# Performance work log

Measured on AMD Instinct MI355X. Metric: run time of the kernel, lower is better.

The kernel has to match this reference:

```python
import jax, jax.numpy as jnp
import numpy as np

N_NODES = 100_000
N_EDGES = 1_600_000
N_GRAPHS = 1024
IN_CH = 5
EPS_BN = 1e-5


def _p(key, shape, scale=0.1):
    return scale * jax.random.normal(key, shape, dtype=jnp.float32)


def setup_inputs() -> dict:
    key = jax.random.key(0)
    ks = jax.random.split(key, 24)
    x = jax.random.normal(ks[0], (N_NODES, IN_CH), dtype=jnp.float32)
    edge_index = jax.random.randint(ks[1], (2, N_EDGES), 0, N_NODES, dtype=jnp.int64)
    batch = jnp.sort(jax.random.randint(ks[2], (N_NODES,), 0, N_GRAPHS, dtype=jnp.int64))
    return {
        "x": x, "edge_index": edge_index, "batch": batch,
        "W1": _p(ks[3], (IN_CH, 128)), "a1_src": _p(ks[4], (4, 32)), "a1_dst": _p(ks[5], (4, 32)), "b1": jnp.zeros((128,), jnp.float32),
        "g1": jnp.ones((128,), jnp.float32), "be1": jnp.zeros((128,), jnp.float32),
        "W2": _p(ks[6], (128, 128)), "a2_src": _p(ks[7], (4, 32)), "a2_dst": _p(ks[8], (4, 32)), "b2": jnp.zeros((128,), jnp.float32),
        "g2": jnp.ones((128,), jnp.float32), "be2": jnp.zeros((128,), jnp.float32),
        # conv3: 128 -> 64, 1 head, mean (concat=False)
        "W3": _p(ks[9], (128, 64)), "a3_src": _p(ks[10], (1, 64)), "a3_dst": _p(ks[11], (1, 64)), "b3": jnp.zeros((64,), jnp.float32),
        # classifier Linear(128,64) -> ELU -> Linear(64,1)
        "fc1_w": _p(ks[12], (128, 64)), "fc1_b": jnp.zeros((64,), jnp.float32),
        "fc2_w": _p(ks[13], (64, 1)), "fc2_b": jnp.zeros((1,), jnp.float32),
    }


def _gat_conv(x, src, dst, W, a_src, a_dst, bias, heads, out_ch, concat):
    """PyG GATConv (negative_slope=0.2, self-loops already appended, eval-mode dropout)."""
    n = x.shape[0]
    h = (x @ W).reshape(n, heads, out_ch)                      # [N,H,C]
    al_s = jnp.sum(h * a_src, axis=-1)                         # [N,H]
    al_d = jnp.sum(h * a_dst, axis=-1)                         # [N,H]
    e = jax.nn.leaky_relu(al_s[src] + al_d[dst], 0.2)          # [E,H]
    m = jax.lax.stop_gradient(jax.ops.segment_max(e, dst, num_segments=n))
    p = jnp.exp(e - m[dst])
    s = jax.ops.segment_sum(p, dst, num_segments=n)
    alpha = p / (s[dst] + 1e-16)                               # segment softmax over in-edges of dst
    out = jax.ops.segment_sum(h[src] * alpha[:, :, None], dst, num_segments=n)  # [N,H,C]
    out = out.reshape(n, heads * out_ch) if concat else out.mean(axis=1)
    return out + bias


def _bn(x, g, b):
    mu = x.mean(axis=0)
    var = x.var(axis=0)
    return (x - mu) * jax.lax.rsqrt(var + EPS_BN) * g + b


def reference(x, edge_index, batch,
              W1, a1_src, a1_dst, b1, g1, be1,
              W2, a2_src, a2_dst, b2, g2, be2,
              W3, a3_src, a3_dst, b3,
              fc1_w, fc1_b, fc2_w, fc2_b):
    n = x.shape[0]
    # PyG GATConv default add_self_loops=True
    loops = jnp.arange(n, dtype=edge_index.dtype)
    src = jnp.concatenate([edge_index[0], loops])
    dst = jnp.concatenate([edge_index[1], loops])

    h = jax.nn.elu(_bn(_gat_conv(x, src, dst, W1, a1_src, a1_dst, b1, 4, 32, True), g1, be1))
    h = jax.nn.elu(_bn(_gat_conv(h, src, dst, W2, a2_src, a2_dst, b2, 4, 32, True), g2, be2))
    h = jax.nn.elu(_gat_conv(h, src, dst, W3, a3_src, a3_dst, b3, 1, 64, False))  # [N,64]

    counts = jax.ops.segment_sum(jnp.ones((n,), h.dtype), batch, num_segments=N_GRAPHS)
    mean_p = jax.ops.segment_sum(h, batch, num_segments=N_GRAPHS) / jnp.maximum(counts, 1.0)[:, None]
    max_p = jax.ops.segment_max(h, batch, num_segments=N_GRAPHS)
    max_p = jnp.where(counts[:, None] > 0, max_p, 0.0)
    hg = jnp.concatenate([mean_p, max_p], axis=1)              # [B,128]

    z = jax.nn.elu(hg @ fc1_w + fc1_b)
    return (z @ fc2_w + fc2_b).squeeze(-1)                     # [B]
```

## Files before the change

### kernel.cpp

```cpp
#include <hip/hip_runtime.h>
#include <hip/hip_bf16.h>
#include <hip/hip_fp16.h>


#define BSHIFT 7
#define BCAP 4096
#define BUCKCAP 2560
#define SCH 32

typedef __attribute__((ext_vector_type(8))) _Float16 half8;
typedef __attribute__((ext_vector_type(4))) float f32x4;

__device__ __forceinline__ float leaky02(float e) { return e > 0.f ? e : 0.2f * e; }

__device__ __forceinline__ unsigned short f16u(float x) {
    __half h = __float2half_rn(x);
    return *(unsigned short*)&h;
}
__device__ __forceinline__ unsigned pack_h2(float a, float b) {
    __half2 h = __floats2half2_rn(a, b);
    return *(unsigned*)&h;
}
__device__ __forceinline__ float2 h2f2(unsigned u) {
    __half2 h = *(__half2*)&u;
    return __half22float2(h);
}

__global__ __launch_bounds__(256) void k_bscatter(const int* __restrict__ src,
                                                  const int* __restrict__ dst,
                                                  int* __restrict__ cursor,
                                                  uint2* __restrict__ ebuf, int E, int nb) {
    __shared__ int hist[1024];
    __shared__ int baseArr[1024];
    int tid = threadIdx.x;
    int chunk0 = blockIdx.x * (256 * SCH);
    for (int i = tid; i < nb; i += 256) hist[i] = 0;
    __syncthreads();
    int rank[SCH];
#pragma unroll
    for (int it = 0; it < SCH; it++) {
        int e = chunk0 + it * 256 + tid;
        rank[it] = (e < E) ? atomicAdd(&hist[dst[e] >> BSHIFT], 1) : 0;
    }
    __syncthreads();
    for (int b = tid; b < nb; b += 256) {
        int c = hist[b];
        baseArr[b] = c ? atomicAdd(&cursor[b], c) : 0;
    }
    __syncthreads();
#pragma unroll
    for (int it = 0; it < SCH; it++) {
        int e = chunk0 + it * 256 + tid;
        if (e < E) {
            int d = dst[e];
            int bk = d >> BSHIFT;
            int local = baseArr[bk] + rank[it];
            if (local < BUCKCAP)
                ebuf[(size_t)bk * BUCKCAP + local] = make_uint2((unsigned)d, (unsigned)src[e]);
        }
    }
}

__global__ __launch_bounds__(256) void k_bsort(const uint2* __restrict__ ebuf,
                                               const int* __restrict__ cursor,
                                               int2* __restrict__ rowInfo,
                                               int* __restrict__ colv, int N) {
    int b = blockIdx.x;
    int base = b * BUCKCAP;
    int count = cursor[b];
    if (count > BUCKCAP) count = BUCKCAP;
    int tid = threadIdx.x;
    __shared__ int hist[128], scanin[128], hist2[128];
    __shared__ int lrank[BCAP];
    __shared__ int lsrc[BCAP];
    if (tid < 128) { hist[tid] = 0; hist2[tid] = 0; }
    __syncthreads();
    bool staged = (count <= BCAP);
    for (int i = tid; i < count; i += 256) {
        uint2 p = ebuf[base + i];
        int local = p.x & 127;
        int r = atomicAdd(&hist[local], 1);
        if (staged) lrank[i] = (r << 7) | local;
    }
    __syncthreads();
    if (tid < 128) scanin[tid] = hist[tid];
    __syncthreads();
#pragma unroll
    for (int off = 1; off < 128; off <<= 1) {
        int v = 0;
        if (tid < 128 && tid >= off) v = scanin[tid - off];
        __syncthreads();
        if (tid < 128) scanin[tid] += v;
        __syncthreads();
    }
    int nodeBase = b << BSHIFT;
    if (tid < 128) {
        int n = nodeBase + tid;
        if (n < N) {
            int beg = base + scanin[tid] - hist[tid];
            rowInfo[n] = make_int2(beg, beg + hist[tid]);
        }
    }
    __syncthreads();
    if (staged) {
        for (int i = tid; i < count; i += 256) {
            uint2 p = ebuf[base + i];
            int lr = lrank[i];
            int local = lr & 127;
            int pos = (scanin[local] - hist[local]) + (lr >> 7);
            lsrc[pos] = (int)p.y;
        }
        __syncthreads();
        for (int i = tid; i < count; i += 256) colv[base + i] = lsrc[i];
    } else {
        for (int i = tid; i < count; i += 256) {
            uint2 p = ebuf[base + i];
            int local = p.x & 127;
            int r = atomicAdd(&hist2[local], 1);
            colv[base + (scanin[local] - hist[local]) + r] = (int)p.y;
        }
    }
}

__global__ __launch_bounds__(256) void k_l1(const float* __restrict__ x, const float* __restrict__ W,
                                            const float* __restrict__ asrc, const float* __restrict__ adst,
                                            unsigned* __restrict__ hb, float* __restrict__ als,
                                            float* __restrict__ ald, int N, int waveBlk,
                                            const float* __restrict__ W2, const float* __restrict__ W3,
                                            unsigned short* __restrict__ Wt2h,
                                            unsigned short* __restrict__ Wt3h) {
    if ((int)blockIdx.x >= waveBlk) {
        int which = blockIdx.x - waveBlk;
        const float* Wsrc = which ? W3 : W2;
        unsigned short* Wdst = which ? Wt3h : Wt2h;
        int sh = which ? 6 : 7;
        int total = 128 << sh;
        int msk = (1 << sh) - 1;
        for (int i = threadIdx.x; i < total; i += 256) {
            int k = i >> sh, n = i & msk;
            Wdst[n * 128 + k] = f16u(Wsrc[i]);
        }
        return;
    }
    int w = (blockIdx.x * blockDim.x + threadIdx.x) >> 6;
    if (w >= N) return;
    int lane = threadIdx.x & 63;
    float xv[5];
#pragma unroll
    for (int k = 0; k < 5; k++) xv[k] = x[(size_t)w * 5 + k];
    int c0 = 2 * lane;
    float h0 = 0.f, h1 = 0.f;
#pragma unroll
    for (int k = 0; k < 5; k++) {
        float2 wv = ((const float2*)(W + k * 128))[lane];
        h0 += xv[k] * wv.x;
        h1 += xv[k] * wv.y;
    }
    hb[(size_t)w * 64 + lane] = pack_h2(h0, h1);
    float s = h0 * asrc[c0] + h1 * asrc[c0 + 1];
    float d = h0 * adst[c0] + h1 * adst[c0 + 1];
#pragma unroll
    for (int off = 1; off <= 8; off <<= 1) { s += __shfl_xor(s, off); d += __shfl_xor(d, off); }
    if ((lane & 15) == 0) {
        int g = lane >> 4;
        als[(size_t)w * 4 + g] = s;
        ald[(size_t)w * 4 + g] = d;
    }
}

__global__ __launch_bounds__(256) void k_agg128(const unsigned* __restrict__ h,
                                                const float* __restrict__ als, const float* __restrict__ ald,
                                                const int2* __restrict__ rowInfo, const int* __restrict__ colv,
                                                const float* __restrict__ bias,
                                                unsigned* __restrict__ out, int N) {
    int w = (blockIdx.x * blockDim.x + threadIdx.x) >> 6;
    if (w >= N) return;
    int lane = threadIdx.x & 63;
    int grp = lane >> 4;
    int l16 = lane & 15;
    int head = l16 >> 2;
    float aldn = ald[(size_t)w * 4 + head];
    float acc[8] = {};
    float dsum = 0.f;

    auto edge = [&](int s) {
        float a = als[(size_t)s * 4 + head];
        float wt = __expf(leaky02(a + aldn));
        uint4 u = *(const uint4*)&h[(size_t)s * 64 + l16 * 4];
        float2 p0 = h2f2(u.x), p1 = h2f2(u.y), p2 = h2f2(u.z), p3 = h2f2(u.w);
        acc[0] += wt * p0.x; acc[1] += wt * p0.y;
        acc[2] += wt * p1.x; acc[3] += wt * p1.y;
        acc[4] += wt * p2.x; acc[5] += wt * p2.y;
        acc[6] += wt * p3.x; acc[7] += wt * p3.y;
        dsum += wt;
    };

    if (grp == 0) edge(w);
    int2 ri = rowInfo[w];
    int p = ri.x + grp, end = ri.y;
    for (; p + 4 < end; p += 8) {
        int s0 = colv[p], s1 = colv[p + 4];
        edge(s0);
        edge(s1);
    }
    if (p < end) edge(colv[p]);

#pragma unroll
    for (int i = 0; i < 8; i++) {
        acc[i] += __shfl_xor(acc[i], 16);
        acc[i] += __shfl_xor(acc[i], 32);
    }
    dsum += __shfl_xor(dsum, 16);
    dsum += __shfl_xor(dsum, 32);

    if (grp == 0) {
        float inv = 1.f / (dsum + 1e-16f);
        const float4* b4 = (const float4*)(bias + 8 * l16);
        float4 bv0 = b4[0], bv1 = b4[1];
        float v[8];
        v[0] = acc[0] * inv + bv0.x; v[1] = acc[1] * inv + bv0.y;
        v[2] = acc[2] * inv + bv0.z; v[3] = acc[3] * inv + bv0.w;
        v[4] = acc[4] * inv + bv1.x; v[5] = acc[5] * inv + bv1.y;
        v[6] = acc[6] * inv + bv1.z; v[7] = acc[7] * inv + bv1.w;
        uint4 o;
        o.x = pack_h2(v[0], v[1]);
        o.y = pack_h2(v[2], v[3]);
        o.z = pack_h2(v[4], v[5]);
        o.w = pack_h2(v[6], v[7]);
        *(uint4*)&out[(size_t)w * 64 + l16 * 4] = o;
    }
}

__global__ __launch_bounds__(256) void k_agg64(const unsigned* __restrict__ h,
                                               const float* __restrict__ als, const float* __restrict__ ald,
                                               const int2* __restrict__ rowInfo, const int* __restrict__ colv,
                                               const float* __restrict__ bias,
                                               unsigned* __restrict__ out, int N) {
    int w = (blockIdx.x * blockDim.x + threadIdx.x) >> 6;
    if (w >= N) return;
    int lane = threadIdx.x & 63;
    int grp = lane >> 3;
    int l8 = lane & 7;
    float aldn = ald[w];
    float acc[8] = {};
    float dsum = 0.f;

    auto edge = [&](int s) {
        float wt = __expf(leaky02(als[s] + aldn));
        uint4 u = *(const uint4*)&h[(size_t)s * 32 + l8 * 4];
        float2 p0 = h2f2(u.x), p1 = h2f2(u.y), p2 = h2f2(u.z), p3 = h2f2(u.w);
        acc[0] += wt * p0.x; acc[1] += wt * p0.y;
        acc[2] += wt * p1.x; acc[3] += wt * p1.y;
        acc[4] += wt * p2.x; acc[5] += wt * p2.y;
        acc[6] += wt * p3.x; acc[7] += wt * p3.y;
        dsum += wt;
    };

    if (grp == 0) edge(w);
    int2 ri = rowInfo[w];
    int p = ri.x + grp, end = ri.y;
    for (; p + 8 < end; p += 16) {
        int s0 = colv[p], s1 = colv[p + 8];
        edge(s0);
        edge(s1);
    }
    if (p < end) edge(colv[p]);

#pragma unroll
    for (int i = 0; i < 8; i++) {
        acc[i] += __shfl_xor(acc[i], 8);
        acc[i] += __shfl_xor(acc[i], 16);
        acc[i] += __shfl_xor(acc[i], 32);
    }
    dsum += __shfl_xor(dsum, 8);
    dsum += __shfl_xor(dsum, 16);
    dsum += __shfl_xor(dsum, 32);

    if (grp == 0) {
        float inv = 1.f / (dsum + 1e-16f);
        const float4* b4 = (const float4*)(bias + 8 * l8);
        float4 bv0 = b4[0], bv1 = b4[1];
        float v[8];
#pragma unroll
        for (int i = 0; i < 8; i++) v[i] = acc[i] * inv;
        v[0] += bv0.x; v[1] += bv0.y; v[2] += bv0.z; v[3] += bv0.w;
        v[4] += bv1.x; v[5] += bv1.y; v[6] += bv1.z; v[7] += bv1.w;
#pragma unroll
        for (int i = 0; i < 8; i++) v[i] = v[i] > 0.f ? v[i] : expm1f(v[i]);
        uint4 o;
        o.x = pack_h2(v[0], v[1]);
        o.y = pack_h2(v[2], v[3]);
        o.z = pack_h2(v[4], v[5]);
        o.w = pack_h2(v[6], v[7]);
        *(uint4*)&out[(size_t)w * 32 + l8 * 4] = o;
    }
}

__global__ __launch_bounds__(256) void k_bnstats_b(const unsigned* __restrict__ x,
                                                   float* __restrict__ stats, int N) {
    __shared__ float lsum[128], lsq[128];
    int tid = threadIdx.x;
    if (tid < 128) { lsum[tid] = 0.f; lsq[tid] = 0.f; }
    __syncthreads();
    int wrd = tid & 63;
    int part = tid >> 6;
    float s0 = 0.f, q0 = 0.f, s1 = 0.f, q1 = 0.f;
    for (int r = blockIdx.x * 4 + part; r < N; r += gridDim.x * 4) {
        float2 v = h2f2(x[(size_t)r * 64 + wrd]);
        s0 += v.x; q0 += v.x * v.x;
        s1 += v.y; q1 += v.y * v.y;
    }
    atomicAdd(&lsum[2 * wrd], s0);
    atomicAdd(&lsum[2 * wrd + 1], s1);
    atomicAdd(&lsq[2 * wrd], q0);
    atomicAdd(&lsq[2 * wrd + 1], q1);
    __syncthreads();
    if (tid < 128) {
        atomicAdd(&stats[tid], lsum[tid]);
        atomicAdd(&stats[128 + tid], lsq[tid]);
    }
}

template <int BN>
__global__ __launch_bounds__(256) void k_gemm_mfma(
        const unsigned* __restrict__ A, const unsigned short* __restrict__ Wt,
        const float* __restrict__ stats, const float* __restrict__ g,
        const float* __restrict__ be,
        unsigned* __restrict__ hb, float* __restrict__ als, float* __restrict__ ald,
        const float* __restrict__ asrc, const float* __restrict__ adst,
        int M, float invN) {
    constexpr int NT = BN / 16;
    __shared__ unsigned short Wlds[BN][136];
    __shared__ unsigned short At[64][136];
    __shared__ float sc[128], sh[128];
    const int tid = threadIdx.x;
    const int wave = tid >> 6, lane = tid & 63;
    const int quad = lane >> 4, l16 = lane & 15;
    const int r0 = blockIdx.x * 64;

    if (tid < 128) {
        float mean = stats[tid] * invN;
        float var = stats[128 + tid] * invN - mean * mean;
        float s = rsqrtf(var + 1e-5f) * g[tid];
        sc[tid] = s;
        sh[tid] = be[tid] - mean * s;
    }
    for (int i = tid; i < BN * 16; i += 256) {
        int n = i >> 4;
        int k8 = (i & 15) * 8;
        uint4 v = *(const uint4*)(Wt + n * 128 + k8);
        *(uint4*)&Wlds[n][k8] = v;
    }
    __syncthreads();
    for (int i = tid; i < 64 * 32; i += 256) {
        int row = i >> 5;
        int p2 = i & 31;
        int c = p2 * 4;
        int r = r0 + row;
        uint2 v = make_uint2(0u, 0u);
        if (r < M) v = *(const uint2*)(A + (size_t)r * 64 + p2 * 2);
        float2 a0 = h2f2(v.x), a1 = h2f2(v.y);
        float t0 = a0.x * sc[c + 0] + sh[c + 0];
        float t1 = a0.y * sc[c + 1] + sh[c + 1];
        float t2 = a1.x * sc[c + 2] + sh[c + 2];
        float t3 = a1.y * sc[c + 3] + sh[c + 3];
        t0 = t0 > 0.f ? t0 : expm1f(t0);
        t1 = t1 > 0.f ? t1 : expm1f(t1);
        t2 = t2 > 0.f ? t2 : expm1f(t2);
        t3 = t3 > 0.f ? t3 : expm1f(t3);
        *(uint2*)&At[row][c] = make_uint2(pack_h2(t0, t1), pack_h2(t2, t3));
    }
    __syncthreads();

    half8 afr[4];
#pragma unroll
    for (int ks = 0; ks < 4; ks++)
        afr[ks] = *(const half8*)&At[wave * 16 + l16][ks * 32 + quad * 8];
    f32x4 acc[NT];
#pragma unroll
    for (int nt = 0; nt < NT; nt++) acc[nt] = (f32x4){0.f, 0.f, 0.f, 0.f};
#pragma unroll
    for (int ks = 0; ks < 4; ks++) {
#pragma unroll
        for (int nt = 0; nt < NT; nt++) {
            half8 bfrag = *(const half8*)&Wlds[nt * 16 + l16][ks * 32 + quad * 8];
            acc[nt] = __builtin_amdgcn_mfma_f32_16x16x32_f16(afr[ks], bfrag, acc[nt], 0, 0, 0);
        }
    }

    float as_[NT], ad_[NT];
#pragma unroll
    for (int nt = 0; nt < NT; nt++) {
        as_[nt] = asrc[nt * 16 + l16];
        ad_[nt] = adst[nt * 16 + l16];
    }

#pragma unroll
    for (int r = 0; r < 4; r++) {
        int gr = r0 + wave * 16 + quad * 4 + r;
        if constexpr (BN == 128) {
            float sv[4] = {0.f, 0.f, 0.f, 0.f}, dv[4] = {0.f, 0.f, 0.f, 0.f};
#pragma unroll
            for (int nt = 0; nt < NT; nt++) {
                float v = acc[nt][r];
                sv[nt >> 1] += v * as_[nt];
                dv[nt >> 1] += v * ad_[nt];
            }
#pragma unroll
            for (int hd = 0; hd < 4; hd++) {
                float s = sv[hd], d = dv[hd];
                s += __shfl_xor(s, 1); s += __shfl_xor(s, 2);
                s += __shfl_xor(s, 4); s += __shfl_xor(s, 8);
                d += __shfl_xor(d, 1); d += __shfl_xor(d, 2);
                d += __shfl_xor(d, 4); d += __shfl_xor(d, 8);
                if (l16 == 0 && gr < M) {
                    als[(size_t)gr * 4 + hd] = s;
                    ald[(size_t)gr * 4 + hd] = d;
                }
            }
        } else {
            float s = 0.f, d = 0.f;
#pragma unroll
            for (int nt = 0; nt < NT; nt++) {
                float v = acc[nt][r];
                s += v * as_[nt];
                d += v * ad_[nt];
            }
            s += __shfl_xor(s, 1); s += __shfl_xor(s, 2);
            s += __shfl_xor(s, 4); s += __shfl_xor(s, 8);
            d += __shfl_xor(d, 1); d += __shfl_xor(d, 2);
            d += __shfl_xor(d, 4); d += __shfl_xor(d, 8);
            if (l16 == 0 && gr < M) { als[gr] = s; ald[gr] = d; }
        }
    }
#pragma unroll
    for (int nt = 0; nt < NT; nt++) {
#pragma unroll
        for (int r = 0; r < 4; r++) {
            float v = acc[nt][r];
            float o = __shfl_xor(v, 1);
            if ((lane & 1) == 0) {
                int gr = r0 + wave * 16 + quad * 4 + r;
                if (gr < M)
                    hb[(size_t)gr * (BN / 2) + nt * 8 + (l16 >> 1)] = pack_h2(v, o);
            }
        }
    }
}

__global__ __launch_bounds__(256) void k_pool(const unsigned* __restrict__ h, const int* __restrict__ batch,
                                              const float* __restrict__ fc1w, const float* __restrict__ fc1b,
                                              const float* __restrict__ fc2w, const float* __restrict__ fc2b,
                                              float* __restrict__ out, int N) {
    int g = blockIdx.x;
    int tid = threadIdx.x;
    int wv = tid >> 6, lane = tid & 63;
    int lo, hi;
    {
        int a = 0, b = N;
        while (a < b) { int m = (a + b) >> 1; if (batch[m] < g) a = m + 1; else b = m; }
        lo = a;
    }
    {
        int a = lo, b = N;
        while (a < b) { int m = (a + b) >> 1; if (batch[m] < g + 1) a = m + 1; else b = m; }
        hi = a;
    }
    int wrd = lane & 31, half = lane >> 5;
    float s0 = 0.f, s1 = 0.f, m0 = -3.4e38f, m1 = -3.4e38f;
    for (int r = lo + wv * 2 + half; r < hi; r += 8) {
        float2 v = h2f2(h[(size_t)r * 32 + wrd]);
        s0 += v.x; s1 += v.y;
        m0 = fmaxf(m0, v.x); m1 = fmaxf(m1, v.y);
    }
    s0 += __shfl_xor(s0, 32);
    s1 += __shfl_xor(s1, 32);
    m0 = fmaxf(m0, __shfl_xor(m0, 32));
    m1 = fmaxf(m1, __shfl_xor(m1, 32));
    __shared__ float ps[4][64], pm[4][64];
    if (half == 0) {
        ps[wv][2 * wrd] = s0;     ps[wv][2 * wrd + 1] = s1;
        pm[wv][2 * wrd] = m0;     pm[wv][2 * wrd + 1] = m1;
    }
    __syncthreads();
    int cnt = hi - lo;
    __shared__ float hg[128];
    if (tid < 64) {
        float sum = ps[0][tid] + ps[1][tid] + ps[2][tid] + ps[3][tid];
        float mx = fmaxf(fmaxf(pm[0][tid], pm[1][tid]), fmaxf(pm[2][tid], pm[3][tid]));
        hg[tid] = sum / fmaxf((float)cnt, 1.f);
        hg[64 + tid] = (cnt > 0) ? mx : 0.f;
    }
    __syncthreads();
    if (wv == 0) {
        float z = fc1b[lane];
        for (int k = 0; k < 128; k++) z += hg[k] * fc1w[k * 64 + lane];
        z = z > 0.f ? z : expm1f(z);
        float o = z * fc2w[lane];
#pragma unroll
        for (int off = 32; off >= 1; off >>= 1) o += __shfl_down(o, off);
        if (lane == 0) out[g] = o + fc2b[0];
    }
}

extern "C" void kernel_launch(void* const* d_in, const int* in_sizes, int n_in,
                              void* d_out, int out_size, void* d_ws, size_t ws_size,
                              hipStream_t stream) {
    const float* x = (const float*)d_in[0];
    const int* ei = (const int*)d_in[1];
    const int* batch = (const int*)d_in[2];
    const float* W1 = (const float*)d_in[3];
    const float* a1s = (const float*)d_in[4];
    const float* a1d = (const float*)d_in[5];
    const float* b1 = (const float*)d_in[6];
    const float* g1 = (const float*)d_in[7];
    const float* be1 = (const float*)d_in[8];
    const float* W2 = (const float*)d_in[9];
    const float* a2s = (const float*)d_in[10];
    const float* a2d = (const float*)d_in[11];
    const float* b2 = (const float*)d_in[12];
    const float* g2 = (const float*)d_in[13];
    const float* be2 = (const float*)d_in[14];
    const float* W3 = (const float*)d_in[15];
    const float* a3s = (const float*)d_in[16];
    const float* a3d = (const float*)d_in[17];
    const float* b3 = (const float*)d_in[18];
    const float* fc1w = (const float*)d_in[19];
    const float* fc1b = (const float*)d_in[20];
    const float* fc2w = (const float*)d_in[21];
    const float* fc2b = (const float*)d_in[22];

    const int N = in_sizes[2];
    const int E = in_sizes[1] / 2;
    const int NG = out_size;
    const int* src = ei;
    const int* dst = ei + E;
    const int nb = (N + 127) >> BSHIFT;

    char* ws = (char*)d_ws;
    size_t off = 0;
    auto alloc = [&](size_t bytes) -> void* {
        void* p = ws + off;
        off += (bytes + 255) / 256 * 256;
        return p;
    };
    unsigned* bufAb = (unsigned*)alloc((size_t)N * 64 * 4);
    unsigned* hb = (unsigned*)alloc((size_t)N * 64 * 4);
    unsigned* h3b = (unsigned*)alloc((size_t)N * 32 * 4);
    uint2* ebuf = (uint2*)alloc((size_t)nb * BUCKCAP * 8);
    int* colArr = (int*)alloc((size_t)nb * BUCKCAP * 4);
    int2* rowInfo = (int2*)alloc((size_t)N * 8);
    float* als = (float*)alloc((size_t)N * 4 * 4);
    float* ald = (float*)alloc((size_t)N * 4 * 4);
    unsigned short* Wt2h = (unsigned short*)alloc(128 * 128 * 2);
    unsigned short* Wt3h = (unsigned short*)alloc(64 * 128 * 2);
    size_t cursorPad = ((size_t)nb * 4 + 255) / 256 * 256;
    int* cursor = (int*)alloc((size_t)nb * 4);
    float* stats = (float*)alloc(512 * 4);

    hipMemsetAsync(cursor, 0, cursorPad + 512 * 4, stream);

    const int waveBlocks = (N * 64 + 255) / 256;
    const int gemmBlocks = (N + 63) / 64;
    const float invN = 1.f / N;

    k_bscatter<<<(E + 256 * SCH - 1) / (256 * SCH), 256, 0, stream>>>(src, dst, cursor, ebuf, E, nb);
    k_bsort<<<nb, 256, 0, stream>>>(ebuf, cursor, rowInfo, colArr, N);

    k_l1<<<waveBlocks + 2, 256, 0, stream>>>(x, W1, a1s, a1d, hb, als, ald, N,
                                             waveBlocks, W2, W3, Wt2h, Wt3h);
    k_agg128<<<waveBlocks, 256, 0, stream>>>(hb, als, ald, rowInfo, colArr, b1, bufAb, N);
    k_bnstats_b<<<512, 256, 0, stream>>>(bufAb, stats, N);

    k_gemm_mfma<128><<<gemmBlocks, 256, 0, stream>>>(bufAb, Wt2h, stats, g1, be1,
                                                     hb, als, ald, a2s, a2d, N, invN);
    k_agg128<<<waveBlocks, 256, 0, stream>>>(hb, als, ald, rowInfo, colArr, b2, bufAb, N);
    k_bnstats_b<<<512, 256, 0, stream>>>(bufAb, stats + 256, N);

    k_gemm_mfma<64><<<gemmBlocks, 256, 0, stream>>>(bufAb, Wt3h, stats + 256, g2, be2,
                                                    hb, als, ald, a3s, a3d, N, invN);
    k_agg64<<<waveBlocks, 256, 0, stream>>>(hb, als, ald, rowInfo, colArr, b3, h3b, N);

    k_pool<<<NG, 256, 0, stream>>>(h3b, batch, fc1w, fc1b, fc2w, fc2b, (float*)d_out, N);
}
```

Before: 525.7 us.

## Merge layer-1 and bucket scatter, pack edges to 32 bits, drop GEMM LDS staging

Merges the edge bucket-scatter kernel into the layer-1 projection kernel so one launch does both. Each edge record is packed into a single 32-bit word (7-bit local dst plus 17-bit src) instead of a uint2, which halves ebuf traffic, and the sort kernel is simplified to a single counting pass. The GEMM kernel now builds its A fragments straight from global memory into registers, with BN and ELU applied in place, which removes the At LDS tile and a barrier. The 17-bit src field assumes fewer than 131072 nodes, which holds for this input.

```diff
diff --git a/kernel.cpp b/kernel.cpp
--- a/kernel.cpp
+++ b/kernel.cpp
@@ -4,9 +4,9 @@
 
 
 #define BSHIFT 7
-#define BCAP 4096
 #define BUCKCAP 2560
 #define SCH 32
+#define SRCMASK 0x1FFFF
 
 typedef __attribute__((ext_vector_type(8))) _Float16 half8;
 typedef __attribute__((ext_vector_type(4))) float f32x4;
@@ -26,42 +26,89 @@
     return __half22float2(h);
 }
 
-__global__ __launch_bounds__(256) void k_bscatter(const int* __restrict__ src,
-                                                  const int* __restrict__ dst,
-                                                  int* __restrict__ cursor,
-                                                  uint2* __restrict__ ebuf, int E, int nb) {
+__global__ __launch_bounds__(256) void k_l1_scatter(
+        const float* __restrict__ x, const float* __restrict__ W,
+        const float* __restrict__ asrc, const float* __restrict__ adst,
+        unsigned* __restrict__ hb, float* __restrict__ als, float* __restrict__ ald,
+        int N, int waveBlk,
+        const float* __restrict__ W2, const float* __restrict__ W3,
+        unsigned short* __restrict__ Wt2h, unsigned short* __restrict__ Wt3h,
+        const int* __restrict__ src, const int* __restrict__ dst,
+        int* __restrict__ cursor, unsigned* __restrict__ ebuf, int E, int nb) {
     __shared__ int hist[1024];
     __shared__ int baseArr[1024];
+    int bid = blockIdx.x;
     int tid = threadIdx.x;
-    int chunk0 = blockIdx.x * (256 * SCH);
-    for (int i = tid; i < nb; i += 256) hist[i] = 0;
-    __syncthreads();
-    int rank[SCH];
-#pragma unroll
-    for (int it = 0; it < SCH; it++) {
-        int e = chunk0 + it * 256 + tid;
-        rank[it] = (e < E) ? atomicAdd(&hist[dst[e] >> BSHIFT], 1) : 0;
-    }
-    __syncthreads();
-    for (int b = tid; b < nb; b += 256) {
-        int c = hist[b];
-        baseArr[b] = c ? atomicAdd(&cursor[b], c) : 0;
-    }
-    __syncthreads();
-#pragma unroll
-    for (int it = 0; it < SCH; it++) {
-        int e = chunk0 + it * 256 + tid;
-        if (e < E) {
-            int d = dst[e];
-            int bk = d >> BSHIFT;
-            int local = baseArr[bk] + rank[it];
-            if (local < BUCKCAP)
-                ebuf[(size_t)bk * BUCKCAP + local] = make_uint2((unsigned)d, (unsigned)src[e]);
-        }
-    }
-}
-
-__global__ __launch_bounds__(256) void k_bsort(const uint2* __restrict__ ebuf,
+    if (bid >= waveBlk + 2) {
+        int chunk0 = (bid - waveBlk - 2) * (256 * SCH);
+        for (int i = tid; i < nb; i += 256) hist[i] = 0;
+        __syncthreads();
+        int rank[SCH];
+#pragma unroll
+        for (int it = 0; it < SCH; it++) {
+            int e = chunk0 + it * 256 + tid;
+            rank[it] = (e < E) ? atomicAdd(&hist[dst[e] >> BSHIFT], 1) : 0;
+        }
+        __syncthreads();
+        for (int b = tid; b < nb; b += 256) {
+            int c = hist[b];
+            baseArr[b] = c ? atomicAdd(&cursor[b], c) : 0;
+        }
+        __syncthreads();
+#pragma unroll
+        for (int it = 0; it < SCH; it++) {
+            int e = chunk0 + it * 256 + tid;
+            if (e < E) {
+                int d = dst[e];
+                int bk = d >> BSHIFT;
+                int local = baseArr[bk] + rank[it];
+                if (local < BUCKCAP)
+                    ebuf[(size_t)bk * BUCKCAP + local] =
+                        ((unsigned)(d & 127) << 17) | (unsigned)src[e];
+            }
+        }
+        return;
+    }
+    if (bid >= waveBlk) {
+        int which = bid - waveBlk;
+        const float* Wsrc = which ? W3 : W2;
+        unsigned short* Wdst = which ? Wt3h : Wt2h;
+        int sh = which ? 6 : 7;
+        int total = 128 << sh;
+        int msk = (1 << sh) - 1;
+        for (int i = tid; i < total; i += 256) {
+            int k = i >> sh, n = i & msk;
+            Wdst[n * 128 + k] = f16u(Wsrc[i]);
+        }
+        return;
+    }
+    int w = (bid * 256 + tid) >> 6;
+    if (w >= N) return;
+    int lane = tid & 63;
+    float xv[5];
+#pragma unroll
+    for (int k = 0; k < 5; k++) xv[k] = x[(size_t)w * 5 + k];
+    int c0 = 2 * lane;
+    float h0 = 0.f, h1 = 0.f;
+#pragma unroll
+    for (int k = 0; k < 5; k++) {
+        float2 wv = ((const float2*)(W + k * 128))[lane];
+        h0 += xv[k] * wv.x;
+        h1 += xv[k] * wv.y;
+    }
+    hb[(size_t)w * 64 + lane] = pack_h2(h0, h1);
+    float s = h0 * asrc[c0] + h1 * asrc[c0 + 1];
+    float d = h0 * adst[c0] + h1 * adst[c0 + 1];
+#pragma unroll
+    for (int off = 1; off <= 8; off <<= 1) { s += __shfl_xor(s, off); d += __shfl_xor(d, off); }
+    if ((lane & 15) == 0) {
+        int g = lane >> 4;
+        als[(size_t)w * 4 + g] = s;
+        ald[(size_t)w * 4 + g] = d;
+    }
+}
+
+__global__ __launch_bounds__(256) void k_bsort(const unsigned* __restrict__ ebuf,
                                                const int* __restrict__ cursor,
                                                int2* __restrict__ rowInfo,
                                                int* __restrict__ colv, int N) {
@@ -71,17 +118,11 @@
     if (count > BUCKCAP) count = BUCKCAP;
     int tid = threadIdx.x;
     __shared__ int hist[128], scanin[128], hist2[128];
-    __shared__ int lrank[BCAP];
-    __shared__ int lsrc[BCAP];
+    __shared__ int lsrc[BUCKCAP];
     if (tid < 128) { hist[tid] = 0; hist2[tid] = 0; }
     __syncthreads();
-    bool staged = (count <= BCAP);
-    for (int i = tid; i < count; i += 256) {
-        uint2 p = ebuf[base + i];
-        int local = p.x & 127;
-        int r = atomicAdd(&hist[local], 1);
-        if (staged) lrank[i] = (r << 7) | local;
-    }
+    for (int i = tid; i < count; i += 256)
+        atomicAdd(&hist[ebuf[base + i] >> 17], 1);
     __syncthreads();
     if (tid < 128) scanin[tid] = hist[tid];
     __syncthreads();
@@ -102,70 +143,14 @@
         }
     }
     __syncthreads();
-    if (staged) {
-        for (int i = tid; i < count; i += 256) {
-            uint2 p = ebuf[base + i];
-            int lr = lrank[i];
-            int local = lr & 127;
-            int pos = (scanin[local] - hist[local]) + (lr >> 7);
-            lsrc[pos] = (int)p.y;
-        }
-        __syncthreads();
-        for (int i = tid; i < count; i += 256) colv[base + i] = lsrc[i];
-    } else {
-        for (int i = tid; i < count; i += 256) {
-            uint2 p = ebuf[base + i];
-            int local = p.x & 127;
-            int r = atomicAdd(&hist2[local], 1);
-            colv[base + (scanin[local] - hist[local]) + r] = (int)p.y;
-        }
-    }
-}
-
-__global__ __launch_bounds__(256) void k_l1(const float* __restrict__ x, const float* __restrict__ W,
-                                            const float* __restrict__ asrc, const float* __restrict__ adst,
-                                            unsigned* __restrict__ hb, float* __restrict__ als,
-                                            float* __restrict__ ald, int N, int waveBlk,
-                                            const float* __restrict__ W2, const float* __restrict__ W3,
-                                            unsigned short* __restrict__ Wt2h,
-                                            unsigned short* __restrict__ Wt3h) {
-    if ((int)blockIdx.x >= waveBlk) {
-        int which = blockIdx.x - waveBlk;
-        const float* Wsrc = which ? W3 : W2;
-        unsigned short* Wdst = which ? Wt3h : Wt2h;
-        int sh = which ? 6 : 7;
-        int total = 128 << sh;
-        int msk = (1 << sh) - 1;
-        for (int i = threadIdx.x; i < total; i += 256) {
-            int k = i >> sh, n = i & msk;
-            Wdst[n * 128 + k] = f16u(Wsrc[i]);
-        }
-        return;
-    }
-    int w = (blockIdx.x * blockDim.x + threadIdx.x) >> 6;
-    if (w >= N) return;
-    int lane = threadIdx.x & 63;
-    float xv[5];
-#pragma unroll
-    for (int k = 0; k < 5; k++) xv[k] = x[(size_t)w * 5 + k];
-    int c0 = 2 * lane;
-    float h0 = 0.f, h1 = 0.f;
-#pragma unroll
-    for (int k = 0; k < 5; k++) {
-        float2 wv = ((const float2*)(W + k * 128))[lane];
-        h0 += xv[k] * wv.x;
-        h1 += xv[k] * wv.y;
-    }
-    hb[(size_t)w * 64 + lane] = pack_h2(h0, h1);
-    float s = h0 * asrc[c0] + h1 * asrc[c0 + 1];
-    float d = h0 * adst[c0] + h1 * adst[c0 + 1];
-#pragma unroll
-    for (int off = 1; off <= 8; off <<= 1) { s += __shfl_xor(s, off); d += __shfl_xor(d, off); }
-    if ((lane & 15) == 0) {
-        int g = lane >> 4;
-        als[(size_t)w * 4 + g] = s;
-        ald[(size_t)w * 4 + g] = d;
-    }
+    for (int i = tid; i < count; i += 256) {
+        unsigned p = ebuf[base + i];
+        int local = p >> 17;
+        int r = atomicAdd(&hist2[local], 1);
+        lsrc[(scanin[local] - hist[local]) + r] = (int)(p & SRCMASK);
+    }
+    __syncthreads();
+    for (int i = tid; i < count; i += 256) colv[base + i] = lsrc[i];
 }
 
 __global__ __launch_bounds__(256) void k_agg128(const unsigned* __restrict__ h,
@@ -331,7 +316,6 @@
         int M, float invN) {
     constexpr int NT = BN / 16;
     __shared__ unsigned short Wlds[BN][136];
-    __shared__ unsigned short At[64][136];
     __shared__ float sc[128], sh[128];
     const int tid = threadIdx.x;
     const int wave = tid >> 6, lane = tid & 63;
@@ -348,34 +332,30 @@
     for (int i = tid; i < BN * 16; i += 256) {
         int n = i >> 4;
         int k8 = (i & 15) * 8;
-        uint4 v = *(const uint4*)(Wt + n * 128 + k8);
-        *(uint4*)&Wlds[n][k8] = v;
-    }
-    __syncthreads();
-    for (int i = tid; i < 64 * 32; i += 256) {
-        int row = i >> 5;
-        int p2 = i & 31;
-        int c = p2 * 4;
-        int r = r0 + row;
-        uint2 v = make_uint2(0u, 0u);
-        if (r < M) v = *(const uint2*)(A + (size_t)r * 64 + p2 * 2);
-        float2 a0 = h2f2(v.x), a1 = h2f2(v.y);
-        float t0 = a0.x * sc[c + 0] + sh[c + 0];
-        float t1 = a0.y * sc[c + 1] + sh[c + 1];
-        float t2 = a1.x * sc[c + 2] + sh[c + 2];
-        float t3 = a1.y * sc[c + 3] + sh[c + 3];
-        t0 = t0 > 0.f ? t0 : expm1f(t0);
-        t1 = t1 > 0.f ? t1 : expm1f(t1);
-        t2 = t2 > 0.f ? t2 : expm1f(t2);
-        t3 = t3 > 0.f ? t3 : expm1f(t3);
-        *(uint2*)&At[row][c] = make_uint2(pack_h2(t0, t1), pack_h2(t2, t3));
-    }
-    __syncthreads();
-
+        *(uint4*)&Wlds[n][k8] = *(const uint4*)(Wt + n * 128 + k8);
+    }
+    __syncthreads();
+
+    int arow = r0 + wave * 16 + l16;
+    bool arowOK = arow < M;
+    const uint4* Arow = (const uint4*)(A + (size_t)arow * 64);
     half8 afr[4];
 #pragma unroll
-    for (int ks = 0; ks < 4; ks++)
-        afr[ks] = *(const half8*)&At[wave * 16 + l16][ks * 32 + quad * 8];
+    for (int ks = 0; ks < 4; ks++) {
+        uint4 v = arowOK ? Arow[ks * 4 + quad] : make_uint4(0u, 0u, 0u, 0u);
+        int c = ks * 32 + quad * 8;
+        float2 f0 = h2f2(v.x), f1 = h2f2(v.y), f2 = h2f2(v.z), f3 = h2f2(v.w);
+        float t[8] = {f0.x, f0.y, f1.x, f1.y, f2.x, f2.y, f3.x, f3.y};
+        half8 a;
+#pragma unroll
+        for (int j = 0; j < 8; j++) {
+            float tv = t[j] * sc[c + j] + sh[c + j];
+            tv = tv > 0.f ? tv : expm1f(tv);
+            a[j] = (_Float16)tv;
+        }
+        afr[ks] = a;
+    }
+
     f32x4 acc[NT];
 #pragma unroll
     for (int nt = 0; nt < NT; nt++) acc[nt] = (f32x4){0.f, 0.f, 0.f, 0.f};
@@ -547,7 +527,7 @@
     unsigned* bufAb = (unsigned*)alloc((size_t)N * 64 * 4);
     unsigned* hb = (unsigned*)alloc((size_t)N * 64 * 4);
     unsigned* h3b = (unsigned*)alloc((size_t)N * 32 * 4);
-    uint2* ebuf = (uint2*)alloc((size_t)nb * BUCKCAP * 8);
+    unsigned* ebuf = (unsigned*)alloc((size_t)nb * BUCKCAP * 4);
     int* colArr = (int*)alloc((size_t)nb * BUCKCAP * 4);
     int2* rowInfo = (int2*)alloc((size_t)N * 8);
     float* als = (float*)alloc((size_t)N * 4 * 4);
@@ -562,13 +542,14 @@
 
     const int waveBlocks = (N * 64 + 255) / 256;
     const int gemmBlocks = (N + 63) / 64;
+    const int sBlocks = (E + 256 * SCH - 1) / (256 * SCH);
     const float invN = 1.f / N;
 
-    k_bscatter<<<(E + 256 * SCH - 1) / (256 * SCH), 256, 0, stream>>>(src, dst, cursor, ebuf, E, nb);
+    k_l1_scatter<<<waveBlocks + 2 + sBlocks, 256, 0, stream>>>(
+        x, W1, a1s, a1d, hb, als, ald, N, waveBlocks,
+        W2, W3, Wt2h, Wt3h, src, dst, cursor, ebuf, E, nb);
     k_bsort<<<nb, 256, 0, stream>>>(ebuf, cursor, rowInfo, colArr, N);
 
-    k_l1<<<waveBlocks + 2, 256, 0, stream>>>(x, W1, a1s, a1d, hb, als, ald, N,
-                                             waveBlocks, W2, W3, Wt2h, Wt3h);
     k_agg128<<<waveBlocks, 256, 0, stream>>>(hb, als, ald, rowInfo, colArr, b1, bufAb, N);
     k_bnstats_b<<<512, 256, 0, stream>>>(bufAb, stats, N);
 
```

Measured after the change: 511.2 us. 1.03x faster.
